# Kernel optimization log

Hardware: AMD Instinct MI355X
Metric: run time of the kernel (lower is better)

Reference implementation:

```python
import jax, jax.numpy as jnp
import numpy as np

KS = 7      # kernel_size
PAD = 3     # padding
G = 8       # groups
CIN = 64    # inplanes
COUT = 64   # outplanes
DD = COUT // G        # channels per group = 8
REL = DD // 2         # rel_size = 4


def group_conv1x1(x, w, b):
    # x: (b, C, H, W), w: (G, out_per_g, in_per_g)
    bsz, c, h, ww = x.shape
    xg = x.reshape(bsz, G, c // G, h, ww)
    y = jnp.einsum('bgihw,goi->bgohw', xg, w).reshape(bsz, -1, h, ww)
    if b is not None:
        y = y + b[None, :, None, None]
    return y


def unfold_windows(xp, h, w):
    # xp: (b, C, h+2*PAD, w+2*PAD) -> (b, C, h, w, KS*KS), window flattened (kh, kw)
    return jnp.stack([xp[:, :, i:i + h, j:j + w]
                      for i in range(KS) for j in range(KS)], axis=-1)


def setup_inputs() -> dict:
    key = jax.random.key(0)
    ks = jax.random.split(key, 8)
    x = jax.random.normal(ks[0], (4, CIN, 56, 56), dtype=jnp.float32)
    wq = jax.random.normal(ks[1], (G, DD, CIN // G), dtype=jnp.float32) * 0.1
    wk = jax.random.normal(ks[2], (G, DD, CIN // G), dtype=jnp.float32) * 0.1
    bk = jax.random.normal(ks[3], (COUT,), dtype=jnp.float32) * 0.1
    wv = jax.random.normal(ks[4], (G, DD, CIN // G), dtype=jnp.float32) * 0.1
    bv = jax.random.normal(ks[5], (COUT,), dtype=jnp.float32) * 0.1
    rel_x = jax.random.normal(ks[6], (REL, KS, 1), dtype=jnp.float32)
    rel_y = jax.random.normal(ks[7], (REL, 1, KS), dtype=jnp.float32)
    return {"x": x, "wq": wq, "wk": wk, "bk": bk, "wv": wv, "bv": bv,
            "rel_x": rel_x, "rel_y": rel_y}


def reference(x, wq, wk, bk, wv, bv, rel_x, rel_y):
    b, d, h, w = x.shape
    q = group_conv1x1(x, wq, None)                      # (b, COUT, h, w)
    x_pad = jnp.pad(x, ((0, 0), (0, 0), (PAD, PAD), (PAD, PAD)))
    k = group_conv1x1(x_pad, wk, bk)
    v = group_conv1x1(x_pad, wv, bv)
    kw = unfold_windows(k, h, w).reshape(b, G, DD, h, w, KS * KS)
    vw = unfold_windows(v, h, w).reshape(b, G, DD, h, w, KS * KS)
    qg = q.reshape(b, G, DD, h, w)
    q_x, q_y = qg[:, :, :REL], qg[:, :, REL:]
    rx = jnp.broadcast_to(rel_x, (REL, KS, KS)).reshape(REL, -1)  # (REL, 49)
    ry = jnp.broadcast_to(rel_y, (REL, KS, KS)).reshape(REL, -1)
    qr = jnp.concatenate([jnp.einsum('bgdhw,dk->bgdhwk', q_x, rx),
                          jnp.einsum('bgdhw,dk->bgdhwk', q_y, ry)], axis=2)
    logits = qg[..., None] * kw + qr                    # (b, G, DD, h, w, 49)
    soft = jax.nn.softmax(logits, axis=-1)
    out = jnp.sum(soft * vw, axis=-1).reshape(b, -1, h, w)
    return out
```

## Files before the change

### kernel.cpp

```cpp
#include <hip/hip_runtime.h>
#include <math.h>

#define KS    7
#define PADW  3
#define H     56
#define W     56
#define HW    (H * W)
#define TILE  8
#define PATCH 14
#define PROW  20
#define PCHN  (PATCH * PROW)

__global__ __launch_bounds__(256, 6) void attn_fused(
    const float* __restrict__ x,
    const float* __restrict__ wq,
    const float* __restrict__ wk,
    const float* __restrict__ bk,
    const float* __restrict__ wv,
    const float* __restrict__ bv,
    const float* __restrict__ rel_x,
    const float* __restrict__ rel_y,
    float* __restrict__ out)
{
    __shared__ float ksm[8 * PCHN];
    __shared__ float vsm[8 * PCHN];

    const int tid  = threadIdx.x;
    const int tile = blockIdx.x;
    const int bz   = blockIdx.y;
    const int b    = bz >> 3;
    const int g    = bz & 7;
    const int c0   = g * 8;

    const int tileY = tile / 7;
    const int tileX = tile - tileY * 7;
    const int h0 = tileY * TILE;
    const int w0 = tileX * TILE;

    const float* wqg = wq + g * 64;
    const float* wkg = wk + g * 64;
    const float* wvg = wv + g * 64;
    const float* xg  = x + (size_t)(b * 64 + c0) * HW;

    if (tid < PATCH * PATCH) {
        const int py = tid / PATCH;
        const int px = tid - py * PATCH;
        const int oy = h0 + py - PADW;
        const int ox = w0 + px - PADW;
        const bool in = (oy >= 0) & (oy < H) & (ox >= 0) & (ox < W);
        const float* xp = xg + oy * W + ox;
        float xv[8];
#pragma unroll
        for (int i = 0; i < 8; ++i)
            xv[i] = in ? xp[i * HW] : 0.f;
        const int dst = py * PROW + px;
#pragma unroll
        for (int dch = 0; dch < 8; ++dch) {
            float ka = bk[c0 + dch];
            float va = bv[c0 + dch];
#pragma unroll
            for (int i = 0; i < 8; ++i) {
                ka = fmaf(xv[i], wkg[dch * 8 + i], ka);
                va = fmaf(xv[i], wvg[dch * 8 + i], va);
            }
            ksm[dch * PCHN + dst] = ka;
            vsm[dch * PCHN + dst] = va;
        }
    }
    __syncthreads();

    const int pix  = tid & 63;
    const int dsel = tid >> 6;
    const int ty   = pix >> 3;
    const int tx   = pix & 7;
    const int h    = h0 + ty;
    const int w    = w0 + tx;

    const float* xcp = xg + h * W + w;
    float xc[8];
#pragma unroll
    for (int i = 0; i < 8; ++i)
        xc[i] = xcp[i * HW];

    const int base = ty * PROW + tx;

#pragma unroll
    for (int half = 0; half < 2; ++half) {
        const int dch = half * 4 + dsel;

        float qv = 0.f;
#pragma unroll
        for (int i = 0; i < 8; ++i)
            qv = fmaf(xc[i], wqg[dch * 8 + i], qv);

        float qvr[7];
#pragma unroll
        for (int i = 0; i < 7; ++i) {
            float r = (half == 0) ? rel_x[dch * 7 + i]
                                  : rel_y[(dch - 4) * 7 + i];
            qvr[i] = qv * r;
        }

        const float* kp = ksm + dch * PCHN + base;
        const float* vp = vsm + dch * PCHN + base;

        float l = 0.f, acc = 0.f;
#pragma unroll
        for (int i = 0; i < 7; ++i) {
#pragma unroll
            for (int j = 0; j < 7; ++j) {
                float addv = (half == 0) ? qvr[i] : qvr[j];
                float e = __expf(fmaf(qv, kp[i * PROW + j], addv));
                l += e;
                acc = fmaf(e, vp[i * PROW + j], acc);
            }
        }

        out[((size_t)(b * 64 + c0 + dch) * H + h) * W + w] = acc / l;
    }
}

extern "C" void kernel_launch(void* const* d_in, const int* in_sizes, int n_in,
                              void* d_out, int out_size, void* d_ws, size_t ws_size,
                              hipStream_t stream) {
    const float* x     = (const float*)d_in[0];
    const float* wq    = (const float*)d_in[1];
    const float* wk    = (const float*)d_in[2];
    const float* bk    = (const float*)d_in[3];
    const float* wv    = (const float*)d_in[4];
    const float* bv    = (const float*)d_in[5];
    const float* rel_x = (const float*)d_in[6];
    const float* rel_y = (const float*)d_in[7];

    dim3 grid(49, 32, 1);
    attn_fused<<<grid, dim3(256), 0, stream>>>(
        x, wq, wk, bk, wv, bv, rel_x, rel_y, (float*)d_out);
}
```

Baseline: 82.33 us.

## Interleave K/V in shared memory as float2 and use native exp2/rcp

Stores K and V together as float2 in a compact 14x14 shared-memory patch per channel, so each window tap fetches both with one 64-bit LDS read instead of two scalar reads. Pre-scales q and the relative-position terms by log2(e) so the softmax can use the hardware exp2 builtin directly, and replaces the final division with a hardware reciprocal. Per-row partial sums are also split to shorten the dependent add chains. The approximate reciprocal and exp2 slightly change rounding, and dropping the padded row stride may change LDS bank-conflict behaviour.

```diff
diff --git a/kernel.cpp b/kernel.cpp
--- a/kernel.cpp
+++ b/kernel.cpp
@@ -8,8 +8,20 @@
 #define HW    (H * W)
 #define TILE  8
 #define PATCH 14
-#define PROW  20
-#define PCHN  (PATCH * PROW)
+#define PPOS  (PATCH * PATCH)
+
+#if __has_builtin(__builtin_amdgcn_exp2f)
+#define EXP2F(x) __builtin_amdgcn_exp2f(x)
+#else
+#define EXP2F(x) exp2f(x)
+#endif
+#if __has_builtin(__builtin_amdgcn_rcpf)
+#define RCPF(x) __builtin_amdgcn_rcpf(x)
+#else
+#define RCPF(x) (1.0f / (x))
+#endif
+
+#define LOG2E 1.44269504088896340736f
 
 __global__ __launch_bounds__(256, 6) void attn_fused(
     const float* __restrict__ x,
@@ -22,8 +34,7 @@
     const float* __restrict__ rel_y,
     float* __restrict__ out)
 {
-    __shared__ float ksm[8 * PCHN];
-    __shared__ float vsm[8 * PCHN];
+    __shared__ float2 kvm[8][PPOS];
 
     const int tid  = threadIdx.x;
     const int tile = blockIdx.x;
@@ -42,7 +53,7 @@
     const float* wvg = wv + g * 64;
     const float* xg  = x + (size_t)(b * 64 + c0) * HW;
 
-    if (tid < PATCH * PATCH) {
+    if (tid < PPOS) {
         const int py = tid / PATCH;
         const int px = tid - py * PATCH;
         const int oy = h0 + py - PADW;
@@ -53,7 +64,6 @@
 #pragma unroll
         for (int i = 0; i < 8; ++i)
             xv[i] = in ? xp[i * HW] : 0.f;
-        const int dst = py * PROW + px;
 #pragma unroll
         for (int dch = 0; dch < 8; ++dch) {
             float ka = bk[c0 + dch];
@@ -63,8 +73,7 @@
                 ka = fmaf(xv[i], wkg[dch * 8 + i], ka);
                 va = fmaf(xv[i], wvg[dch * 8 + i], va);
             }
-            ksm[dch * PCHN + dst] = ka;
-            vsm[dch * PCHN + dst] = va;
+            kvm[dch][tid] = make_float2(ka, va);
         }
     }
     __syncthreads();
@@ -82,7 +91,7 @@
     for (int i = 0; i < 8; ++i)
         xc[i] = xcp[i * HW];
 
-    const int base = ty * PROW + tx;
+    const int base = ty * PATCH + tx;
 
 #pragma unroll
     for (int half = 0; half < 2; ++half) {
@@ -92,31 +101,35 @@
 #pragma unroll
         for (int i = 0; i < 8; ++i)
             qv = fmaf(xc[i], wqg[dch * 8 + i], qv);
+        const float qv2 = qv * LOG2E;
 
-        float qvr[7];
+        float qvr2[7];
 #pragma unroll
         for (int i = 0; i < 7; ++i) {
             float r = (half == 0) ? rel_x[dch * 7 + i]
                                   : rel_y[(dch - 4) * 7 + i];
-            qvr[i] = qv * r;
+            qvr2[i] = qv2 * r;
         }
 
-        const float* kp = ksm + dch * PCHN + base;
-        const float* vp = vsm + dch * PCHN + base;
+        const float2* kp = &kvm[dch][base];
 
         float l = 0.f, acc = 0.f;
 #pragma unroll
         for (int i = 0; i < 7; ++i) {
+            float li = 0.f, ai = 0.f;
 #pragma unroll
             for (int j = 0; j < 7; ++j) {
-                float addv = (half == 0) ? qvr[i] : qvr[j];
-                float e = __expf(fmaf(qv, kp[i * PROW + j], addv));
-                l += e;
-                acc = fmaf(e, vp[i * PROW + j], acc);
+                float2 kv = kp[i * PATCH + j];
+                float addv = (half == 0) ? qvr2[i] : qvr2[j];
+                float e = EXP2F(fmaf(qv2, kv.x, addv));
+                li += e;
+                ai = fmaf(e, kv.y, ai);
             }
+            l += li;
+            acc += ai;
         }
 
-        out[((size_t)(b * 64 + c0 + dch) * H + h) * W + w] = acc / l;
+        out[((size_t)(b * 64 + c0 + dch) * H + h) * W + w] = acc * RCPF(l);
     }
 }
 
```

Result: no change. 82.76 us (+0.5%).
